# Optimization experiments

Measured on AMD Instinct MI355X. Metric: run time of the kernel, lower is better.

Reference implementation:

```python
import jax, jax.numpy as jnp
import numpy as np

N_GRAPHS = 1250
NEG_SLOPE = 0.2

def gat_layer(x, src, dst, W, a_src, a_dst, b, concat):
    # x: [N, Fin]; W: [Fin, H*C]; a_src/a_dst: [H, C]; b: [H*C] or [C]
    N = x.shape[0]
    H, C = a_src.shape
    h = (x @ W).reshape(N, H, C)                      # [N,H,C]
    alpha_s = jnp.sum(h * a_src[None], axis=-1)       # [N,H]
    alpha_d = jnp.sum(h * a_dst[None], axis=-1)       # [N,H]
    e = jax.nn.leaky_relu(alpha_s[src] + alpha_d[dst], NEG_SLOPE)  # [E,H]
    # segment softmax over incoming edges of each target node
    m = jax.ops.segment_max(e, dst, num_segments=N)   # [N,H]
    m = jnp.where(jnp.isfinite(m), m, 0.0)
    ex = jnp.exp(e - m[dst])
    s = jax.ops.segment_sum(ex, dst, num_segments=N)  # [N,H]
    alpha = ex / (s[dst] + 1e-16)                     # [E,H]
    msg = h[src] * alpha[..., None]                   # [E,H,C]
    out = jax.ops.segment_sum(msg, dst, num_segments=N)  # [N,H,C]
    out = out.reshape(N, H * C) if concat else out.mean(axis=1)
    return out + b

def setup_inputs() -> dict:
    key = jax.random.key(0)
    ks = jax.random.split(key, 13)
    N, E = 50000, 100000
    x = jax.random.normal(ks[0], (N, 78), dtype=jnp.float32)
    edge_index = jax.random.randint(ks[1], (2, E), 0, N, dtype=jnp.int64)
    # sorted segment ids -> every graph non-empty (~40 nodes each)
    batch = jnp.sort(jax.random.randint(ks[2], (N,), 0, N_GRAPHS, dtype=jnp.int64))
    g = lambda k, shape, fan: jax.random.normal(k, shape, dtype=jnp.float32) / np.float32(np.sqrt(fan))
    return {
        'x': x, 'edge_index': edge_index, 'batch': batch,
        'W1': g(ks[3], (78, 780), 78), 'a_src1': g(ks[4], (10, 78), 78), 'a_dst1': g(ks[5], (10, 78), 78),
        'b1': jnp.zeros((780,), jnp.float32),
        'W2': g(ks[6], (780, 128), 780), 'a_src2': g(ks[7], (1, 128), 128), 'a_dst2': g(ks[8], (1, 128), 128),
        'b2': jnp.zeros((128,), jnp.float32),
        'fc_w': g(ks[9], (128, 128), 128), 'fc_b': jnp.zeros((128,), jnp.float32),
    }

def reference(x, edge_index, batch, W1, a_src1, a_dst1, b1, W2, a_src2, a_dst2, b2, fc_w, fc_b):
    N = x.shape[0]
    loop = jnp.arange(N, dtype=edge_index.dtype)
    src = jnp.concatenate([edge_index[0], loop])  # add self loops (PyG default)
    dst = jnp.concatenate([edge_index[1], loop])
    # dropout layers are identity in eval mode
    h = jax.nn.elu(gat_layer(x, src, dst, W1, a_src1, a_dst1, b1, concat=True))   # [N,780]
    h = jax.nn.relu(gat_layer(h, src, dst, W2, a_src2, a_dst2, b2, concat=True))  # [N,128]
    g = jax.ops.segment_max(h, batch, num_segments=N_GRAPHS)                      # [G,128]
    g = jnp.where(jnp.isfinite(g), g, 0.0)
    return jax.nn.relu(g @ fc_w + fc_b)
```

## Files before the change

### kernel.cpp

```cpp
#include <hip/hip_runtime.h>
#include <hip/hip_bf16.h>
#include <cstdint>

#define CAP 32
typedef __hip_bfloat16 bf16;
typedef __attribute__((ext_vector_type(8))) short short8;
typedef __attribute__((ext_vector_type(4))) float f32x4;

__device__ __forceinline__ float sb2f(short s) {
  unsigned int u = ((unsigned int)(unsigned short)s) << 16;
  return __uint_as_float(u);
}
__device__ __forceinline__ short f2sb(float f) {
  bf16 h = __float2bfloat16(f);
  return *reinterpret_cast<short*>(&h);
}

__global__ void k_detect(const int* __restrict__ ei, int* __restrict__ flag) {
  __shared__ int any;
  if (threadIdx.x == 0) any = 0;
  __syncthreads();
  int v = 0;
  for (int i = 1 + 2 * threadIdx.x; i < 2000; i += 512) v |= ei[i];
  if (v) atomicOr(&any, 1);
  __syncthreads();
  if (threadIdx.x == 0) flag[0] = (any == 0) ? 1 : 0;
}

__device__ __forceinline__ void edge_sd(const int* __restrict__ ei, int e, int f,
                                        int& src, int& dst) {
  if (e < 100000) {
    if (f) { src = ei[2 * e]; dst = ei[200000 + 2 * e]; }
    else   { src = ei[e];     dst = ei[100000 + e]; }
  } else { src = dst = e - 100000; }
  src = min(max(src, 0), 49999);
  dst = min(max(dst, 0), 49999);
}

__global__ void k_prep(const float* __restrict__ x, const float* __restrict__ W1,
                       const float* __restrict__ W2, const float* __restrict__ aw1,
                       const float* __restrict__ dw1, bf16* __restrict__ xb,
                       bf16* __restrict__ W1t, bf16* __restrict__ W2t,
                       bf16* __restrict__ Wat, float* __restrict__ zp, int zeroWords) {
  int i = blockIdx.x * 256 + threadIdx.x;
  if (i < zeroWords) zp[i] = 0.f;
  const int n_xb = 50000 * 96;
  const int n_w1 = 832 * 96;
  const int n_w2 = 128 * 832;
  const int n_wa = 32 * 96;
  if (i < n_xb) {
    int r = i / 96, k = i - r * 96;
    xb[i] = __float2bfloat16(k < 78 ? x[r * 78 + k] : 0.f);
  } else if (i < n_xb + n_w1) {
    int j = i - n_xb;
    int n = j / 96, k = j - n * 96;
    W1t[j] = __float2bfloat16((k < 78 && n < 780) ? W1[k * 780 + n] : 0.f);
  } else if (i < n_xb + n_w1 + n_w2) {
    int j = i - n_xb - n_w1;
    int c = j / 832, k = j - c * 832;
    W2t[j] = __float2bfloat16(k < 780 ? W2[k * 128 + c] : 0.f);
  } else if (i < n_xb + n_w1 + n_w2 + n_wa) {
    int j = i - n_xb - n_w1 - n_w2;
    int c = j / 96, k = j - c * 96;
    float s = 0.f;
    if (k < 78 && c < 20) {
      const float* w = (c < 10) ? aw1 : dw1;
      int h = (c < 10) ? c : c - 10;
      const float* wrow = W1 + k * 780 + h * 78;
      const float* arow = w + h * 78;
      for (int q = 0; q < 78; q++) s += wrow[q] * arow[q];
    }
    Wat[c * 96 + k] = __float2bfloat16(s);
  }
}

__global__ __launch_bounds__(256) void k_gemm1(const bf16* __restrict__ xb,
                                               const bf16* __restrict__ W1t,
                                               const bf16* __restrict__ Wat,
                                               bf16* __restrict__ H1,
                                               float* __restrict__ as1,
                                               float* __restrict__ ad1) {
  __shared__ __align__(16) short Als[64 * 104];
  __shared__ __align__(16) short Bls[64 * 104];
  __shared__ __align__(16) short Wls[32 * 104];
  __shared__ __align__(16) float Cls[64 * 68];
  const int t = threadIdx.x;
  const int w = t >> 6, l = t & 63, l15 = l & 15, q = l >> 4;
  const int rowBase = blockIdx.x * 64;
  for (int s = t; s < 768; s += 256) {
    int row = s / 12, kg = s - row * 12;
    short8 v = {};
    int gr = rowBase + row;
    if (gr < 50000) v = *(const short8*)((const short*)xb + (size_t)gr * 96 + kg * 8);
    *(short8*)&Als[row * 104 + kg * 8] = v;
  }
  for (int s = t; s < 384; s += 256) {
    int row = s / 12, kg = s - row * 12;
    *(short8*)&Wls[row * 104 + kg * 8] =
        *(const short8*)((const short*)Wat + (size_t)row * 96 + kg * 8);
  }
  short8 breg[3];
  int bn[3], bk[3];
#pragma unroll
  for (int i = 0; i < 3; i++) {
    int s = t + i * 256;
    bn[i] = s / 12; bk[i] = s - bn[i] * 12;
    breg[i] = *(const short8*)((const short*)W1t + (size_t)bn[i] * 96 + bk[i] * 8);
  }
  for (int cc = 0; cc < 13; cc++) {
    __syncthreads();
#pragma unroll
    for (int i = 0; i < 3; i++) *(short8*)&Bls[bn[i] * 104 + bk[i] * 8] = breg[i];
    if (cc < 12) {
#pragma unroll
      for (int i = 0; i < 3; i++)
        breg[i] = *(const short8*)((const short*)W1t +
                                   (size_t)((cc + 1) * 64 + bn[i]) * 96 + bk[i] * 8);
    }
    __syncthreads();
    f32x4 acc[4] = {};
#pragma unroll
    for (int ks = 0; ks < 3; ks++) {
      short8 a = *(const short8*)&Als[(w * 16 + l15) * 104 + ks * 32 + q * 8];
#pragma unroll
      for (int nt = 0; nt < 4; nt++) {
        short8 b = *(const short8*)&Bls[(nt * 16 + l15) * 104 + ks * 32 + q * 8];
        acc[nt] = __builtin_amdgcn_mfma_f32_16x16x32_bf16(a, b, acc[nt], 0, 0, 0);
      }
    }
    __syncthreads();
#pragma unroll
    for (int nt = 0; nt < 4; nt++)
#pragma unroll
      for (int r = 0; r < 4; r++)
        Cls[(w * 16 + q * 4 + r) * 68 + nt * 16 + l15] = acc[nt][r];
    __syncthreads();
    {
      int r = t >> 2, c0 = (t & 3) * 16;
      int gr = rowBase + r;
      if (gr < 50000) {
        short8 o0, o1;
#pragma unroll
        for (int c = 0; c < 8; c++) o0[c] = f2sb(Cls[r * 68 + c0 + c]);
#pragma unroll
        for (int c = 0; c < 8; c++) o1[c] = f2sb(Cls[r * 68 + c0 + 8 + c]);
        short* dst = (short*)H1 + (size_t)gr * 832 + cc * 64 + c0;
        *(short8*)dst = o0;
        *(short8*)(dst + 8) = o1;
      }
    }
  }
  f32x4 acc2[2] = {};
#pragma unroll
  for (int ks = 0; ks < 3; ks++) {
    short8 a = *(const short8*)&Als[(w * 16 + l15) * 104 + ks * 32 + q * 8];
#pragma unroll
    for (int nt = 0; nt < 2; nt++) {
      short8 b = *(const short8*)&Wls[(nt * 16 + l15) * 104 + ks * 32 + q * 8];
      acc2[nt] = __builtin_amdgcn_mfma_f32_16x16x32_bf16(a, b, acc2[nt], 0, 0, 0);
    }
  }
  const int gr0 = rowBase + w * 16 + q * 4;
#pragma unroll
  for (int nt = 0; nt < 2; nt++) {
    int c = nt * 16 + l15;
#pragma unroll
    for (int r = 0; r < 4; r++) {
      int gr = gr0 + r;
      if (gr < 50000) {
        if (c < 10)       as1[gr * 10 + c] = acc2[nt][r];
        else if (c < 20)  ad1[gr * 10 + (c - 10)] = acc2[nt][r];
      }
    }
  }
}

__global__ void k_scatter(const int* __restrict__ ei, const int* __restrict__ flag,
                          int* __restrict__ cnt, int* __restrict__ csr) {
  int e = blockIdx.x * 256 + threadIdx.x;
  if (e >= 150000) return;
  int f = flag[0], src, dst;
  edge_sd(ei, e, f, src, dst);
  int pos = atomicAdd(&cnt[dst], 1);
  if (pos < CAP) csr[dst * CAP + pos] = src;
}

__global__ __launch_bounds__(256) void k_agg1(const bf16* __restrict__ H1,
                                              const float* __restrict__ as1,
                                              const float* __restrict__ ad1,
                                              const int* __restrict__ csr,
                                              const int* __restrict__ cnt,
                                              const float* __restrict__ b1,
                                              bf16* __restrict__ HL2) {
  __shared__ float sexw[2][CAP * 10];
  __shared__ float sden[2][16];
  __shared__ int ssrc[2][CAP];
  const int t = threadIdx.x;
  const int sub = t >> 7, tt = t & 127;
  const int n = blockIdx.x * 2 + sub;
  if (tt < 16) sden[sub][tt] = 0.f;
  __syncthreads();
  const int cn = min(cnt[n], CAP);
  for (int wv = tt; wv < cn * 10; wv += 128) {
    int k = wv / 10, h = wv - k * 10;
    int src = csr[n * CAP + k];
    if (h == 0) ssrc[sub][k] = src;
    float e = as1[src * 10 + h] + ad1[n * 10 + h];
    e = e >= 0.f ? e : 0.2f * e;
    float ex = __expf(e);
    sexw[sub][wv] = ex;
    atomicAdd(&sden[sub][h], ex);
  }
  __syncthreads();
  if (tt < 104) {
    int hj[8];
    float bb[8];
#pragma unroll
    for (int c = 0; c < 8; c++) {
      int j = tt * 8 + c;
      int h = j / 78;
      hj[c] = h > 9 ? 9 : h;
      bb[c] = (j < 780) ? b1[j] : 0.f;
    }
    float acc[8] = {};
    const float* sw = sexw[sub];
    const short* H1s = (const short*)H1;
    for (int k = 0; k < cn; k++) {
      int src = ssrc[sub][k];
      short8 hv = *(const short8*)(H1s + (size_t)src * 832 + tt * 8);
      const float* swk = sw + k * 10;
#pragma unroll
      for (int c = 0; c < 8; c++) acc[c] += swk[hj[c]] * sb2f(hv[c]);
    }
    short8 ov;
#pragma unroll
    for (int c = 0; c < 8; c++) {
      float v = acc[c] / (sden[sub][hj[c]] + 1e-16f) + bb[c];
      v = v > 0.f ? v : __expf(v) - 1.f;
      ov[c] = f2sb(v);
    }
    *(short8*)((short*)HL2 + (size_t)n * 832 + tt * 8) = ov;
  }
}

__global__ __launch_bounds__(256) void k_gemm2(const bf16* __restrict__ A,
                                               const bf16* __restrict__ W2t,
                                               const float* __restrict__ AW2,
                                               const float* __restrict__ DW2,
                                               bf16* __restrict__ H2,
                                               float* __restrict__ as2,
                                               float* __restrict__ ad2) {
  __shared__ __align__(16) short Als[64 * 72];
  __shared__ __align__(16) short Bls[128 * 72];
  __shared__ float sAW[128], sDW[128];
  __shared__ float sS[4][64], sD[4][64];
  const int t = threadIdx.x;
  const int w = t >> 6, l = t & 63, l15 = l & 15, q = l >> 4;
  const int rowBase = blockIdx.x * 64;
  if (t < 128) sAW[t] = AW2[t];
  else         sDW[t - 128] = DW2[t - 128];
  const int ar = t >> 2, ak = t & 3;
  short8 areg[2], breg[4];
  {
    int gr0 = rowBase + ar;
#pragma unroll
    for (int i = 0; i < 2; i++) {
      short8 v = {};
      if (gr0 < 50000)
        v = *(const short8*)((const short*)A + (size_t)gr0 * 832 + (ak * 2 + i) * 8);
      areg[i] = v;
    }
#pragma unroll
    for (int i = 0; i < 4; i++) {
      int s = t + i * 256;
      int col = s >> 3, kg = s & 7;
      breg[i] = *(const short8*)((const short*)W2t + (size_t)col * 832 + kg * 8);
    }
  }
  f32x4 acc[4][2] = {};
  for (int kb = 0; kb < 832; kb += 64) {
    __syncthreads();
#pragma unroll
    for (int i = 0; i < 2; i++)
      *(short8*)&Als[ar * 72 + (ak * 2 + i) * 8] = areg[i];
#pragma unroll
    for (int i = 0; i < 4; i++) {
      int s = t + i * 256;
      int col = s >> 3, kg = s & 7;
      *(short8*)&Bls[col * 72 + kg * 8] = breg[i];
    }
    if (kb < 768) {
      int kn = kb + 64;
      int gr = rowBase + ar;
#pragma unroll
      for (int i = 0; i < 2; i++) {
        short8 v = {};
        if (gr < 50000)
          v = *(const short8*)((const short*)A + (size_t)gr * 832 + kn + (ak * 2 + i) * 8);
        areg[i] = v;
      }
#pragma unroll
      for (int i = 0; i < 4; i++) {
        int s = t + i * 256;
        int col = s >> 3, kg = s & 7;
        breg[i] = *(const short8*)((const short*)W2t + (size_t)col * 832 + kn + kg * 8);
      }
    }
    __syncthreads();
#pragma unroll
    for (int ks = 0; ks < 2; ks++) {
      short8 a[4];
#pragma unroll
      for (int mt = 0; mt < 4; mt++)
        a[mt] = *(const short8*)&Als[(mt * 16 + l15) * 72 + ks * 32 + q * 8];
#pragma unroll
      for (int ntl = 0; ntl < 2; ntl++) {
        short8 b = *(const short8*)&Bls[((w * 2 + ntl) * 16 + l15) * 72 + ks * 32 + q * 8];
#pragma unroll
        for (int mt = 0; mt < 4; mt++)
          acc[mt][ntl] = __builtin_amdgcn_mfma_f32_16x16x32_bf16(a[mt], b, acc[mt][ntl], 0, 0, 0);
      }
    }
  }
  const int col0 = w * 32 + l15, col1 = col0 + 16;
  const float aw0 = sAW[col0], aw1 = sAW[col1];
  const float dw0 = sDW[col0], dw1 = sDW[col1];
  f32x4 sp[4], dp[4];
#pragma unroll
  for (int mt = 0; mt < 4; mt++) {
    sp[mt] = acc[mt][0] * aw0 + acc[mt][1] * aw1;
    dp[mt] = acc[mt][0] * dw0 + acc[mt][1] * dw1;
  }
#pragma unroll
  for (int m = 1; m < 16; m <<= 1) {
#pragma unroll
    for (int mt = 0; mt < 4; mt++)
#pragma unroll
      for (int r = 0; r < 4; r++) {
        sp[mt][r] += __shfl_xor(sp[mt][r], m, 64);
        dp[mt][r] += __shfl_xor(dp[mt][r], m, 64);
      }
  }
  if (l15 == 0) {
#pragma unroll
    for (int mt = 0; mt < 4; mt++)
#pragma unroll
      for (int r = 0; r < 4; r++) {
        sS[w][mt * 16 + q * 4 + r] = sp[mt][r];
        sD[w][mt * 16 + q * 4 + r] = dp[mt][r];
      }
  }
#pragma unroll
  for (int mt = 0; mt < 4; mt++) {
    int gr0 = rowBase + mt * 16 + q * 4;
#pragma unroll
    for (int ntl = 0; ntl < 2; ntl++) {
      int gc = w * 32 + ntl * 16 + l15;
#pragma unroll
      for (int r = 0; r < 4; r++) {
        int gr = gr0 + r;
        if (gr < 50000) H2[(size_t)gr * 128 + gc] = __float2bfloat16(acc[mt][ntl][r]);
      }
    }
  }
  __syncthreads();
  if (t < 64) {
    int gr = rowBase + t;
    if (gr < 50000) as2[gr] = sS[0][t] + sS[1][t] + sS[2][t] + sS[3][t];
  } else if (t < 128) {
    int r2 = t - 64;
    int gr = rowBase + r2;
    if (gr < 50000) ad2[gr] = sD[0][r2] + sD[1][r2] + sD[2][r2] + sD[3][r2];
  }
}

__global__ __launch_bounds__(256) void k_agg2(const bf16* __restrict__ H2,
                                              const float* __restrict__ as2,
                                              const float* __restrict__ ad2,
                                              const int* __restrict__ csr,
                                              const int* __restrict__ cnt,
                                              const float* __restrict__ b2,
                                              const int* __restrict__ batch,
                                              const int* __restrict__ flag,
                                              float* __restrict__ g) {
  __shared__ int ssrc[2][CAP];
  __shared__ float sexw[2][CAP];
  __shared__ float sden[2];
  const int t = threadIdx.x;
  const int sub = t >> 7, tt = t & 127;
  const int n = blockIdx.x * 2 + sub;
  if (tt == 0) sden[sub] = 0.f;
  __syncthreads();
  const int cn = min(cnt[n], CAP);
  if (tt < cn) {
    int src = csr[n * CAP + tt];
    ssrc[sub][tt] = src;
    float e = as2[src] + ad2[n];
    e = e >= 0.f ? e : 0.2f * e;
    float ex = __expf(e);
    sexw[sub][tt] = ex;
    atomicAdd(&sden[sub], ex);
  }
  __syncthreads();
  const short* H2s = (const short*)H2;
  float acc = 0.f;
  for (int k = 0; k < cn; k++)
    acc += sexw[sub][k] * sb2f(H2s[(size_t)ssrc[sub][k] * 128 + tt]);
  float v = acc / (sden[sub] + 1e-16f) + b2[tt];
  v = v > 0.f ? v : 0.f;
  int b = flag[0] ? batch[2 * n] : batch[n];
  b = min(max(b, 0), 1249);
  atomicMax((int*)&g[b * 128 + tt], __float_as_int(v));
}

__global__ __launch_bounds__(128) void k_fc(const float* __restrict__ g,
                                            const float* __restrict__ fw,
                                            const float* __restrict__ fb,
                                            float* __restrict__ out) {
  const int n = blockIdx.x, t = threadIdx.x;
  __shared__ float grow[128];
  grow[t] = g[n * 128 + t];
  __syncthreads();
  float acc = fb[t];
  for (int k = 0; k < 128; k++) acc += grow[k] * fw[k * 128 + t];
  out[n * 128 + t] = acc > 0.f ? acc : 0.f;
}

extern "C" void kernel_launch(void* const* d_in, const int* in_sizes, int n_in,
                              void* d_out, int out_size, void* d_ws, size_t ws_size,
                              hipStream_t stream) {
  const float* x     = (const float*)d_in[0];
  const int*   ei    = (const int*)d_in[1];
  const int*   batch = (const int*)d_in[2];
  const float* W1    = (const float*)d_in[3];
  const float* as1w  = (const float*)d_in[4];
  const float* ad1w  = (const float*)d_in[5];
  const float* b1    = (const float*)d_in[6];
  const float* W2    = (const float*)d_in[7];
  const float* as2w  = (const float*)d_in[8];
  const float* ad2w  = (const float*)d_in[9];
  const float* b2    = (const float*)d_in[10];
  const float* fcw   = (const float*)d_in[11];
  const float* fcb   = (const float*)d_in[12];
  float* out = (float*)d_out;

  char* p = (char*)d_ws;
  size_t off = 0;
  auto alloc = [&](size_t bytes) -> void* {
    void* r = p + off;
    off = (off + bytes + 15) & ~(size_t)15;
    return r;
  };
  int*   cnt = (int*)  alloc(50000 * 4);
  float* g   = (float*)alloc(160000 * 4);
  size_t zeroWords = off / 4;
  float* as1 = (float*)alloc(500000 * 4);
  float* ad1 = (float*)alloc(500000 * 4);
  float* as2 = (float*)alloc(50000 * 4);
  float* ad2 = (float*)alloc(50000 * 4);
  bf16*  W1t = (bf16*) alloc((size_t)832 * 96 * 2);
  bf16*  W2t = (bf16*) alloc((size_t)128 * 832 * 2);
  bf16*  Wat = (bf16*) alloc((size_t)32 * 96 * 2);
  bf16*  h1  = (bf16*) alloc((size_t)50000 * 832 * 2);
  bf16*  hl2 = (bf16*) alloc((size_t)50000 * 832 * 2);
  int*   csr = (int*)  alloc((size_t)50000 * CAP * 4);
  void*  uni = alloc((size_t)50000 * 128 * 2);
  bf16*  xb  = (bf16*)uni;
  bf16*  h2  = (bf16*)uni;
  int*   flag = (int*) alloc(16);
  (void)ws_size; (void)in_sizes; (void)n_in; (void)out_size;

  k_detect<<<1, 256, 0, stream>>>(ei, flag);
  int prepN = 50000 * 96 + 832 * 96 + 128 * 832 + 32 * 96;
  k_prep<<<(prepN + 255) / 256, 256, 0, stream>>>(
      x, W1, W2, as1w, ad1w, xb, W1t, W2t, Wat, (float*)d_ws, (int)zeroWords);

  k_gemm1<<<782, 256, 0, stream>>>(xb, W1t, Wat, h1, as1, ad1);
  k_scatter<<<(150000 + 255) / 256, 256, 0, stream>>>(ei, flag, cnt, csr);
  k_agg1<<<25000, 256, 0, stream>>>(h1, as1, ad1, csr, cnt, b1, hl2);
  k_gemm2<<<782, 256, 0, stream>>>(hl2, W2t, as2w, ad2w, h2, as2, ad2);
  k_agg2<<<25000, 256, 0, stream>>>(h2, as2, ad2, csr, cnt, b2, batch, flag, g);
  k_fc<<<1250, 128, 0, stream>>>(g, fcw, fcb, out);
}
```

Measured before the change: 329.0 us.

## Aggregate raw inputs per head before projecting, dropping the materialized H1

Layer 1 aggregation is reordered using linearity: for each head, neighbor rows of the 78-wide input x are softmax-weighted and summed first, then multiplied by that head's 78x78 weight slice with MFMA. This removes writing and re-reading the 50000x832 bf16 H1 intermediate and the full first GEMM. In exchange each head re-gathers neighbor x rows (10 passes over the edges), and the attention logits are computed by a separate small alpha kernel. The pad columns of hl2 are now zeroed in prep.

```diff
diff --git a/kernel.cpp b/kernel.cpp
--- a/kernel.cpp
+++ b/kernel.cpp
@@ -40,27 +40,25 @@
 __global__ void k_prep(const float* __restrict__ x, const float* __restrict__ W1,
                        const float* __restrict__ W2, const float* __restrict__ aw1,
                        const float* __restrict__ dw1, bf16* __restrict__ xb,
-                       bf16* __restrict__ W1t, bf16* __restrict__ W2t,
-                       bf16* __restrict__ Wat, float* __restrict__ zp, int zeroWords) {
+                       bf16* __restrict__ W2t, bf16* __restrict__ Wat,
+                       bf16* __restrict__ W1bd, bf16* __restrict__ hl2,
+                       float* __restrict__ zp, int zeroWords) {
   int i = blockIdx.x * 256 + threadIdx.x;
   if (i < zeroWords) zp[i] = 0.f;
   const int n_xb = 50000 * 96;
-  const int n_w1 = 832 * 96;
   const int n_w2 = 128 * 832;
   const int n_wa = 32 * 96;
+  const int n_bd = 10 * 80 * 96;
+  const int n_pad = 50000 * 52;
   if (i < n_xb) {
     int r = i / 96, k = i - r * 96;
     xb[i] = __float2bfloat16(k < 78 ? x[r * 78 + k] : 0.f);
-  } else if (i < n_xb + n_w1) {
+  } else if (i < n_xb + n_w2) {
     int j = i - n_xb;
-    int n = j / 96, k = j - n * 96;
-    W1t[j] = __float2bfloat16((k < 78 && n < 780) ? W1[k * 780 + n] : 0.f);
-  } else if (i < n_xb + n_w1 + n_w2) {
-    int j = i - n_xb - n_w1;
     int c = j / 832, k = j - c * 832;
     W2t[j] = __float2bfloat16(k < 780 ? W2[k * 128 + c] : 0.f);
-  } else if (i < n_xb + n_w1 + n_w2 + n_wa) {
-    int j = i - n_xb - n_w1 - n_w2;
+  } else if (i < n_xb + n_w2 + n_wa) {
+    int j = i - n_xb - n_w2;
     int c = j / 96, k = j - c * 96;
     float s = 0.f;
     if (k < 78 && c < 20) {
@@ -71,19 +69,25 @@
       for (int q = 0; q < 78; q++) s += wrow[q] * arow[q];
     }
     Wat[c * 96 + k] = __float2bfloat16(s);
-  }
-}
-
-__global__ __launch_bounds__(256) void k_gemm1(const bf16* __restrict__ xb,
-                                               const bf16* __restrict__ W1t,
+  } else if (i < n_xb + n_w2 + n_wa + n_bd) {
+    int j = i - n_xb - n_w2 - n_wa;
+    int hh = j / (80 * 96);
+    int rem = j - hh * 80 * 96;
+    int jj = rem / 96, k = rem - jj * 96;
+    W1bd[j] = __float2bfloat16((jj < 78 && k < 78) ? W1[k * 780 + hh * 78 + jj] : 0.f);
+  } else if (i < n_xb + n_w2 + n_wa + n_bd + n_pad) {
+    int j = i - n_xb - n_w2 - n_wa - n_bd;
+    int r = j / 52, c = j - r * 52;
+    hl2[(size_t)r * 832 + 780 + c] = __float2bfloat16(0.f);
+  }
+}
+
+__global__ __launch_bounds__(256) void k_alpha(const bf16* __restrict__ xb,
                                                const bf16* __restrict__ Wat,
-                                               bf16* __restrict__ H1,
                                                float* __restrict__ as1,
                                                float* __restrict__ ad1) {
   __shared__ __align__(16) short Als[64 * 104];
-  __shared__ __align__(16) short Bls[64 * 104];
   __shared__ __align__(16) short Wls[32 * 104];
-  __shared__ __align__(16) float Cls[64 * 68];
   const int t = threadIdx.x;
   const int w = t >> 6, l = t & 63, l15 = l & 15, q = l >> 4;
   const int rowBase = blockIdx.x * 64;
@@ -99,57 +103,7 @@
     *(short8*)&Wls[row * 104 + kg * 8] =
         *(const short8*)((const short*)Wat + (size_t)row * 96 + kg * 8);
   }
-  short8 breg[3];
-  int bn[3], bk[3];
-#pragma unroll
-  for (int i = 0; i < 3; i++) {
-    int s = t + i * 256;
-    bn[i] = s / 12; bk[i] = s - bn[i] * 12;
-    breg[i] = *(const short8*)((const short*)W1t + (size_t)bn[i] * 96 + bk[i] * 8);
-  }
-  for (int cc = 0; cc < 13; cc++) {
-    __syncthreads();
-#pragma unroll
-    for (int i = 0; i < 3; i++) *(short8*)&Bls[bn[i] * 104 + bk[i] * 8] = breg[i];
-    if (cc < 12) {
-#pragma unroll
-      for (int i = 0; i < 3; i++)
-        breg[i] = *(const short8*)((const short*)W1t +
-                                   (size_t)((cc + 1) * 64 + bn[i]) * 96 + bk[i] * 8);
-    }
-    __syncthreads();
-    f32x4 acc[4] = {};
-#pragma unroll
-    for (int ks = 0; ks < 3; ks++) {
-      short8 a = *(const short8*)&Als[(w * 16 + l15) * 104 + ks * 32 + q * 8];
-#pragma unroll
-      for (int nt = 0; nt < 4; nt++) {
-        short8 b = *(const short8*)&Bls[(nt * 16 + l15) * 104 + ks * 32 + q * 8];
-        acc[nt] = __builtin_amdgcn_mfma_f32_16x16x32_bf16(a, b, acc[nt], 0, 0, 0);
-      }
-    }
-    __syncthreads();
-#pragma unroll
-    for (int nt = 0; nt < 4; nt++)
-#pragma unroll
-      for (int r = 0; r < 4; r++)
-        Cls[(w * 16 + q * 4 + r) * 68 + nt * 16 + l15] = acc[nt][r];
-    __syncthreads();
-    {
-      int r = t >> 2, c0 = (t & 3) * 16;
-      int gr = rowBase + r;
-      if (gr < 50000) {
-        short8 o0, o1;
-#pragma unroll
-        for (int c = 0; c < 8; c++) o0[c] = f2sb(Cls[r * 68 + c0 + c]);
-#pragma unroll
-        for (int c = 0; c < 8; c++) o1[c] = f2sb(Cls[r * 68 + c0 + 8 + c]);
-        short* dst = (short*)H1 + (size_t)gr * 832 + cc * 64 + c0;
-        *(short8*)dst = o0;
-        *(short8*)(dst + 8) = o1;
-      }
-    }
-  }
+  __syncthreads();
   f32x4 acc2[2] = {};
 #pragma unroll
   for (int ks = 0; ks < 3; ks++) {
@@ -185,61 +139,100 @@
   if (pos < CAP) csr[dst * CAP + pos] = src;
 }
 
-__global__ __launch_bounds__(256) void k_agg1(const bf16* __restrict__ H1,
-                                              const float* __restrict__ as1,
-                                              const float* __restrict__ ad1,
-                                              const int* __restrict__ csr,
-                                              const int* __restrict__ cnt,
-                                              const float* __restrict__ b1,
-                                              bf16* __restrict__ HL2) {
-  __shared__ float sexw[2][CAP * 10];
-  __shared__ float sden[2][16];
-  __shared__ int ssrc[2][CAP];
+__global__ __launch_bounds__(256) void k_gemmbd(const bf16* __restrict__ xb,
+                                                const bf16* __restrict__ W1bd,
+                                                const float* __restrict__ as1,
+                                                const float* __restrict__ ad1,
+                                                const int* __restrict__ csr,
+                                                const int* __restrict__ cnt,
+                                                const float* __restrict__ b1,
+                                                bf16* __restrict__ HL2) {
+  __shared__ __align__(16) short Als[64 * 104];
+  __shared__ __align__(16) short Bls[80 * 104];
+  __shared__ __align__(16) float Cls[64 * 84];
   const int t = threadIdx.x;
-  const int sub = t >> 7, tt = t & 127;
-  const int n = blockIdx.x * 2 + sub;
-  if (tt < 16) sden[sub][tt] = 0.f;
-  __syncthreads();
-  const int cn = min(cnt[n], CAP);
-  for (int wv = tt; wv < cn * 10; wv += 128) {
-    int k = wv / 10, h = wv - k * 10;
-    int src = csr[n * CAP + k];
-    if (h == 0) ssrc[sub][k] = src;
-    float e = as1[src * 10 + h] + ad1[n * 10 + h];
-    e = e >= 0.f ? e : 0.2f * e;
-    float ex = __expf(e);
-    sexw[sub][wv] = ex;
-    atomicAdd(&sden[sub][h], ex);
-  }
-  __syncthreads();
-  if (tt < 104) {
-    int hj[8];
-    float bb[8];
+  const int h = blockIdx.y;
+  const int rowBase = blockIdx.x * 64;
+#pragma unroll
+  for (int i = 0; i < 4; i++) {
+    int s = t + i * 256;
+    if (s < 960) {
+      int row = s / 12, kg = s - row * 12;
+      *(short8*)&Bls[row * 104 + kg * 8] =
+          *(const short8*)((const short*)W1bd + ((size_t)h * 80 + row) * 96 + kg * 8);
+    }
+  }
+  {
+    const int row = t >> 2, part = t & 3, co = part * 24;
+    const int n = rowBase + row;
+    float acc[24];
+#pragma unroll
+    for (int c = 0; c < 24; c++) acc[c] = 0.f;
+    float den = 0.f;
+    if (n < 50000) {
+      const int cn = min(cnt[n], CAP);
+      const float adn = ad1[n * 10 + h];
+      const short* xs = (const short*)xb;
+      for (int k = 0; k < cn; k++) {
+        int src = csr[n * CAP + k];
+        float e = as1[src * 10 + h] + adn;
+        e = e >= 0.f ? e : 0.2f * e;
+        float wgt = __expf(e);
+        den += wgt;
+        const short* xr = xs + (size_t)src * 96 + co;
+        short8 v0 = *(const short8*)(xr);
+        short8 v1 = *(const short8*)(xr + 8);
+        short8 v2 = *(const short8*)(xr + 16);
+#pragma unroll
+        for (int c = 0; c < 8; c++) {
+          acc[c]      += wgt * sb2f(v0[c]);
+          acc[8 + c]  += wgt * sb2f(v1[c]);
+          acc[16 + c] += wgt * sb2f(v2[c]);
+        }
+      }
+    }
+    float sc = 1.f / (den + 1e-16f);
+    short8 o0, o1, o2;
 #pragma unroll
     for (int c = 0; c < 8; c++) {
-      int j = tt * 8 + c;
-      int h = j / 78;
-      hj[c] = h > 9 ? 9 : h;
-      bb[c] = (j < 780) ? b1[j] : 0.f;
-    }
-    float acc[8] = {};
-    const float* sw = sexw[sub];
-    const short* H1s = (const short*)H1;
-    for (int k = 0; k < cn; k++) {
-      int src = ssrc[sub][k];
-      short8 hv = *(const short8*)(H1s + (size_t)src * 832 + tt * 8);
-      const float* swk = sw + k * 10;
-#pragma unroll
-      for (int c = 0; c < 8; c++) acc[c] += swk[hj[c]] * sb2f(hv[c]);
-    }
-    short8 ov;
-#pragma unroll
-    for (int c = 0; c < 8; c++) {
-      float v = acc[c] / (sden[sub][hj[c]] + 1e-16f) + bb[c];
-      v = v > 0.f ? v : __expf(v) - 1.f;
-      ov[c] = f2sb(v);
-    }
-    *(short8*)((short*)HL2 + (size_t)n * 832 + tt * 8) = ov;
+      o0[c] = f2sb(acc[c] * sc);
+      o1[c] = f2sb(acc[8 + c] * sc);
+      o2[c] = f2sb(acc[16 + c] * sc);
+    }
+    *(short8*)&Als[row * 104 + co]      = o0;
+    *(short8*)&Als[row * 104 + co + 8]  = o1;
+    *(short8*)&Als[row * 104 + co + 16] = o2;
+  }
+  __syncthreads();
+  const int w = t >> 6, l = t & 63, l15 = l & 15, q = l >> 4;
+  f32x4 cacc[5] = {};
+#pragma unroll
+  for (int ks = 0; ks < 3; ks++) {
+    short8 a = *(const short8*)&Als[(w * 16 + l15) * 104 + ks * 32 + q * 8];
+#pragma unroll
+    for (int nt = 0; nt < 5; nt++) {
+      short8 b = *(const short8*)&Bls[(nt * 16 + l15) * 104 + ks * 32 + q * 8];
+      cacc[nt] = __builtin_amdgcn_mfma_f32_16x16x32_bf16(a, b, cacc[nt], 0, 0, 0);
+    }
+  }
+#pragma unroll
+  for (int nt = 0; nt < 5; nt++)
+#pragma unroll
+    for (int r = 0; r < 4; r++)
+      Cls[(w * 16 + q * 4 + r) * 84 + nt * 16 + l15] = cacc[nt][r];
+  __syncthreads();
+  for (int j = t; j < 64 * 39; j += 256) {
+    int r = j / 39, c2 = j - r * 39;
+    int gr = rowBase + r;
+    if (gr < 50000) {
+      int gc = c2 * 2;
+      float v0 = Cls[r * 84 + gc]     + b1[h * 78 + gc];
+      float v1 = Cls[r * 84 + gc + 1] + b1[h * 78 + gc + 1];
+      v0 = v0 > 0.f ? v0 : __expf(v0) - 1.f;
+      v1 = v1 > 0.f ? v1 : __expf(v1) - 1.f;
+      short2 o; o.x = f2sb(v0); o.y = f2sb(v1);
+      *(short2*)((short*)HL2 + (size_t)gr * 832 + h * 78 + gc) = o;
+    }
   }
 }
 
@@ -454,16 +447,15 @@
   int*   cnt = (int*)  alloc(50000 * 4);
   float* g   = (float*)alloc(160000 * 4);
   size_t zeroWords = off / 4;
-  float* as1 = (float*)alloc(500000 * 4);
-  float* ad1 = (float*)alloc(500000 * 4);
-  float* as2 = (float*)alloc(50000 * 4);
-  float* ad2 = (float*)alloc(50000 * 4);
-  bf16*  W1t = (bf16*) alloc((size_t)832 * 96 * 2);
-  bf16*  W2t = (bf16*) alloc((size_t)128 * 832 * 2);
-  bf16*  Wat = (bf16*) alloc((size_t)32 * 96 * 2);
-  bf16*  h1  = (bf16*) alloc((size_t)50000 * 832 * 2);
-  bf16*  hl2 = (bf16*) alloc((size_t)50000 * 832 * 2);
-  int*   csr = (int*)  alloc((size_t)50000 * CAP * 4);
+  float* as1  = (float*)alloc(500000 * 4);
+  float* ad1  = (float*)alloc(500000 * 4);
+  float* as2  = (float*)alloc(50000 * 4);
+  float* ad2  = (float*)alloc(50000 * 4);
+  bf16*  W2t  = (bf16*) alloc((size_t)128 * 832 * 2);
+  bf16*  Wat  = (bf16*) alloc((size_t)32 * 96 * 2);
+  bf16*  W1bd = (bf16*) alloc((size_t)10 * 80 * 96 * 2);
+  bf16*  hl2  = (bf16*) alloc((size_t)50000 * 832 * 2);
+  int*   csr  = (int*)  alloc((size_t)50000 * CAP * 4);
   void*  uni = alloc((size_t)50000 * 128 * 2);
   bf16*  xb  = (bf16*)uni;
   bf16*  h2  = (bf16*)uni;
@@ -471,13 +463,13 @@
   (void)ws_size; (void)in_sizes; (void)n_in; (void)out_size;
 
   k_detect<<<1, 256, 0, stream>>>(ei, flag);
-  int prepN = 50000 * 96 + 832 * 96 + 128 * 832 + 32 * 96;
+  int prepN = 50000 * 96 + 128 * 832 + 32 * 96 + 10 * 80 * 96 + 50000 * 52;
   k_prep<<<(prepN + 255) / 256, 256, 0, stream>>>(
-      x, W1, W2, as1w, ad1w, xb, W1t, W2t, Wat, (float*)d_ws, (int)zeroWords);
-
-  k_gemm1<<<782, 256, 0, stream>>>(xb, W1t, Wat, h1, as1, ad1);
+      x, W1, W2, as1w, ad1w, xb, W2t, Wat, W1bd, hl2, (float*)d_ws, (int)zeroWords);
+
+  k_alpha<<<782, 256, 0, stream>>>(xb, Wat, as1, ad1);
   k_scatter<<<(150000 + 255) / 256, 256, 0, stream>>>(ei, flag, cnt, csr);
-  k_agg1<<<25000, 256, 0, stream>>>(h1, as1, ad1, csr, cnt, b1, hl2);
+  k_gemmbd<<<dim3(782, 10), 256, 0, stream>>>(xb, W1bd, as1, ad1, csr, cnt, b1, hl2);
   k_gemm2<<<782, 256, 0, stream>>>(hl2, W2t, as2w, ad2w, h2, as2, ad2);
   k_agg2<<<25000, 256, 0, stream>>>(h2, as2, ad2, csr, cnt, b2, batch, flag, g);
   k_fc<<<1250, 128, 0, stream>>>(g, fcw, fcb, out);
```

Result: faster. 321.0 us (-2.4%).
